# Kernel tuning notes

Measured on AMD Instinct MI355X. Metric: run time of the kernel, lower is better.

Reference implementation:

```python
import jax, jax.numpy as jnp
import numpy as np

EPS = 1e-5
MIN_NORM = 1e-10

def _norm(x):
    return jnp.sqrt(jnp.clip(jnp.sum(x * x, axis=-1, keepdims=True), MIN_NORM, None))

def _proj(x):
    # clip points to the open unit Poincare ball
    n = _norm(x)
    max_n = 1.0 - EPS
    return jnp.where(n > max_n, x * (max_n / n), x)

def _artanh(x):
    return jnp.arctanh(jnp.clip(x, -1.0 + EPS, 1.0 - EPS))

def mob_add(u, v):
    uv = jnp.sum(u * v, axis=-1, keepdims=True)
    u2 = jnp.sum(u * u, axis=-1, keepdims=True)
    v2 = jnp.sum(v * v, axis=-1, keepdims=True)
    num = (1.0 + 2.0 * uv + v2) * u + (1.0 - u2) * v
    den = 1.0 + 2.0 * uv + u2 * v2
    return _proj(num / jnp.maximum(den, MIN_NORM))

def mob_mat_mul(M, x):
    # M: [Din, Dout], x: [B, Din] on the ball. Ganea Mobius matvec.
    x = _proj(x)
    Mx = x @ M
    x_n = _norm(x)
    Mx_n = _norm(Mx)
    return _proj(jnp.tanh(Mx_n / x_n * _artanh(x_n)) * (Mx / Mx_n))

def log_map_zero(y):
    n = _norm(y)
    return _artanh(n) * y / n

def exp_map_zero(v):
    n = _norm(v)
    return _proj(jnp.tanh(n) * v / n)

def mob_pointwise_prod(x, u):
    # coordinate-wise scale of hyperbolic x by gate u, in the tangent space at 0
    return exp_map_zero(log_map_zero(x) * u)

def _transition(W, h, U, x, b):
    Wh = mob_mat_mul(W, h)
    Ux = mob_mat_mul(U, x)
    return mob_add(mob_add(Wh, Ux), b)

def setup_inputs() -> dict:
    B, I, H = 2048, 1024, 1024
    Din, Dh = 2 * I, 2 * H
    k = (1.0 / H) ** 0.5
    key = jax.random.key(0)
    ks = jax.random.split(key, 8)
    return {
        "hyp_x": jax.random.normal(ks[0], (B, Din), jnp.float32) * 0.01,
        "hidden": jax.random.normal(ks[1], (B, Dh), jnp.float32) * 0.01,
        "w_z": jax.random.uniform(ks[2], (Dh, Dh), jnp.float32, -k, k),
        "w_r": jax.random.uniform(ks[3], (Dh, Dh), jnp.float32, -k, k),
        "w_h": jax.random.uniform(ks[4], (Dh, Dh), jnp.float32, -k, k),
        "u_z": jax.random.uniform(ks[5], (Din, Dh), jnp.float32, -k, k),
        "u_r": jax.random.uniform(ks[6], (Din, Dh), jnp.float32, -k, k),
        "b_z": jnp.zeros((Dh,), jnp.float32),
        "b_r": jnp.zeros((Dh,), jnp.float32),
        "b_h": jnp.zeros((Dh,), jnp.float32),
    }

def reference(hyp_x, hidden, w_z, w_r, w_h, u_z, u_r, b_z, b_r, b_h):
    hyp_x = _proj(hyp_x)
    hidden = _proj(hidden)
    z = jax.nn.sigmoid(log_map_zero(_transition(w_z, hidden, u_z, hyp_x, b_z)))
    r = jax.nn.sigmoid(log_map_zero(_transition(w_r, hidden, u_r, hyp_x, b_r)))
    r_point_h = mob_pointwise_prod(hidden, r)
    # NOTE: original source uses u_r (not u_h) here; replicated faithfully.
    h_tilde = _transition(w_h, r_point_h, u_r, hyp_x, b_h)
    minus_h_oplus_htilde = mob_add(-hidden, h_tilde)
    new_h = mob_add(hidden, mob_pointwise_prod(minus_h_oplus_htilde, z))
    return new_h
```

## Files before the change

kernel.cpp:

```cpp
#include <hip/hip_runtime.h>
#include <hip/hip_bf16.h>
#include <math.h>

#define EPS 1e-5f
#define MAXN (1.0f - EPS)
#define MINN 1e-10f

constexpr int D = 2048;

typedef unsigned short u16;
typedef __bf16 bf16x8 __attribute__((ext_vector_type(8)));
typedef float floatx4 __attribute__((ext_vector_type(4)));


__device__ __forceinline__ u16 f2bf(float f) {
    union { float f; unsigned u; } v; v.f = f;
    unsigned r = v.u + 0x7FFFu + ((v.u >> 16) & 1u);
    return (u16)(r >> 16);
}

__device__ __forceinline__ float bf2f(u16 b) {
    union { unsigned u; float f; } v; v.u = ((unsigned)b) << 16; return v.f;
}

__device__ __forceinline__ void load_bf8(const u16* p, float* d) {
    uint4 r = *(const uint4*)p;
    unsigned w[4] = {r.x, r.y, r.z, r.w};
    #pragma unroll
    for (int i = 0; i < 4; ++i) {
        d[2 * i]     = bf2f((u16)(w[i] & 0xFFFFu));
        d[2 * i + 1] = bf2f((u16)(w[i] >> 16));
    }
}

__device__ __forceinline__ void store_bf8(u16* p, const float* s) {
    u16 pk[8];
    #pragma unroll
    for (int i = 0; i < 8; ++i) pk[i] = f2bf(s[i]);
    *(uint4*)p = *(const uint4*)pk;
}

__device__ __forceinline__ void load_f8(const float* p, float* d) {
    *(float4*)(d)     = *(const float4*)(p);
    *(float4*)(d + 4) = *(const float4*)(p + 4);
}

__device__ __forceinline__ void store_f8(float* p, const float* s) {
    *(float4*)(p)     = *(const float4*)(s);
    *(float4*)(p + 4) = *(const float4*)(s + 4);
}

__device__ __forceinline__ float artanh_(float x) {
    x = fminf(fmaxf(x, -1.0f + EPS), 1.0f - EPS);
    return 0.5f * logf((1.0f + x) / (1.0f - x));
}

__device__ __forceinline__ float sigmoid_(float x) {
    return 1.0f / (1.0f + expf(-x));
}

__device__ __forceinline__ void gl_lds16(const u16* g, u16* l) {
    __builtin_amdgcn_global_load_lds(
        (const __attribute__((address_space(1))) unsigned int*)g,
        (__attribute__((address_space(3))) unsigned int*)l, 16, 0, 0);
}

template<int N>
__device__ __forceinline__ void block_sums(float* v, float* sbuf) {
    #pragma unroll
    for (int n = 0; n < N; ++n)
        #pragma unroll
        for (int off = 32; off >= 1; off >>= 1) v[n] += __shfl_xor(v[n], off, 64);
    int w = threadIdx.x >> 6;
    __syncthreads();
    if ((threadIdx.x & 63) == 0) {
        #pragma unroll
        for (int n = 0; n < N; ++n) sbuf[w * N + n] = v[n];
    }
    __syncthreads();
    #pragma unroll
    for (int n = 0; n < N; ++n)
        v[n] = sbuf[n] + sbuf[N + n] + sbuf[2 * N + n] + sbuf[3 * N + n];
}

__device__ __forceinline__ void mmm_finish(float sum2, float g, float* coef, float* onorm) {
    float mxn = sqrtf(fmaxf(sum2, MINN));
    float tt  = tanhf(mxn * g);
    float on  = fminf(tt, MAXN);
    *coef = on / mxn;
    *onorm = on;
}

__device__ __forceinline__ float mob_apply(float* u, const float* v,
                                           float u2, float v2, float duv) {
    float cu  = 1.f + 2.f * duv + v2;
    float cv  = 1.f - u2;
    float den = fmaxf(1.f + 2.f * duv + u2 * v2, MINN);
    float s2  = cu * cu * u2 + 2.f * cu * cv * duv + cv * cv * v2;
    float n   = sqrtf(fmaxf(s2 / (den * den), MINN));
    float sc  = ((n > MAXN) ? MAXN / n : 1.f) / den;
    #pragma unroll
    for (int i = 0; i < 8; ++i) u[i] = sc * (cu * u[i] + cv * v[i]);
    return fminf(n, MAXN);
}

__device__ __forceinline__ void trans_tile(const float* W, u16* Wt,
                                           int n0, int k0, float* tile) {
    int t = threadIdx.x;
    int lr = t >> 4, lc = (t & 15) * 4;
    #pragma unroll
    for (int p = 0; p < 4; ++p) {
        int r = lr + p * 16;
        float4 v = *(const float4*)(W + (size_t)(k0 + r) * D + n0 + lc);
        tile[r * 65 + lc + 0] = v.x;
        tile[r * 65 + lc + 1] = v.y;
        tile[r * 65 + lc + 2] = v.z;
        tile[r * 65 + lc + 3] = v.w;
    }
    __syncthreads();
    int wn = t >> 3, ws = (t & 7) * 8;
    #pragma unroll
    for (int p = 0; p < 2; ++p) {
        int n = wn + p * 32;
        u16 pk[8];
        #pragma unroll
        for (int j = 0; j < 8; ++j) pk[j] = f2bf(tile[(ws + j) * 65 + n]);
        *(uint4*)(Wt + (size_t)(n0 + n) * D + k0 + ws) = *(uint4*)pk;
    }
}


struct PrepBatch {
    const float* W[5]; u16* Wt[5];
    const float* hx; const float* h;
    u16* hx_bf; u16* h_bf;
    float* g_x; float* g_h;
};

__global__ __launch_bounds__(256) void wtrans_prep(PrepBatch pb) {
    __shared__ float tile[64 * 65];
    int t = threadIdx.x;

    if (blockIdx.z != 4) {
        int wi = (blockIdx.z == 5) ? 4 : blockIdx.z;
        trans_tile(pb.W[wi], pb.Wt[wi],
                   blockIdx.x * 64, blockIdx.y * 64, tile);
    } else {
        int bid = blockIdx.y * (D / 64) + blockIdx.x;
        for (int rr = 0; rr < 2; ++rr) {
            int b = bid * 2 + rr;
            size_t off = (size_t)b * D + t * 8;
            float xv[8], hv[8];
            load_f8(pb.hx + off, xv);
            load_f8(pb.h + off, hv);
            float s[2] = {0.f, 0.f};
            #pragma unroll
            for (int i = 0; i < 8; ++i) { s[0] += xv[i] * xv[i]; s[1] += hv[i] * hv[i]; }
            block_sums<2>(s, tile);

            float nx = sqrtf(fmaxf(s[0], MINN));
            float scx = (nx > MAXN) ? MAXN / nx : 1.0f;
            float nh = sqrtf(fmaxf(s[1], MINN));
            float sch = (nh > MAXN) ? MAXN / nh : 1.0f;
            #pragma unroll
            for (int i = 0; i < 8; ++i) { xv[i] *= scx; hv[i] *= sch; }
            store_bf8(pb.hx_bf + off, xv);
            store_bf8(pb.h_bf + off, hv);
            if (t == 0) {
                float xn = fminf(nx, MAXN), hn = fminf(nh, MAXN);
                pb.g_x[b] = artanh_(xn) / xn;
                pb.g_h[b] = artanh_(hn) / hn;
            }
        }
    }
}


#define PHASE_MID() do { \
    __builtin_amdgcn_s_barrier(); \
    __builtin_amdgcn_s_setprio(1); } while (0)

#define PHASE_END() do { \
    __builtin_amdgcn_s_setprio(0); \
    __builtin_amdgcn_s_barrier(); } while (0)

template<int KLEN, int NJ>
__device__ __forceinline__ void gemm256_body(const u16* __restrict__ A,
                                             const u16* __restrict__ W,
                                             u16* __restrict__ C, int koff,
                                             u16* As, u16* Ws) {
    constexpr int T  = KLEN / 64;
    constexpr int BN = NJ * 64;
    constexpr int AU = 8192;
    constexpr int BU = BN * 32;

    int t0 = threadIdx.x;
    int wave = t0 >> 6, lane = t0 & 63, l16 = lane & 15, quad = lane >> 4;
    int wr = wave >> 2, wc = wave & 3;
    int brow = blockIdx.y * 256, bcol = blockIdx.x * BN;

    int srow = t0 >> 2;
    int sseg = (t0 & 3) ^ ((srow >> 1) & 3);
    const u16* srcA = A + (size_t)(brow + srow) * D + koff + sseg * 8;
    const u16* srcB = W + (size_t)(bcol + srow) * D + koff + sseg * 8;
    u16* ldsA = As + wave * 512;
    u16* ldsB = Ws + wave * 512;

    auto stageA = [&](int buf, int kh, int tile) {
        const u16* s = srcA + tile * 64 + kh * 32;
        u16* d = ldsA + (buf * 2 + kh) * AU;
        gl_lds16(s, d);
        gl_lds16(s + (size_t)128 * D, d + 4096);
    };
    auto stageB = [&](int buf, int kh, int tile) {
        const u16* s = srcB + tile * 64 + kh * 32;
        u16* d = ldsB + (buf * 2 + kh) * BU;
        gl_lds16(s, d);
        if constexpr (NJ == 4) gl_lds16(s + (size_t)128 * D, d + 4096);
    };

    const u16* aF = As + (wr * 128 + l16) * 32 + ((quad ^ ((l16 >> 1) & 3)) * 8);
    const u16* bF = Ws + (wc * (NJ * 16) + l16) * 32 + ((quad ^ ((l16 >> 1) & 3)) * 8);

    floatx4 acc[8][NJ];
    #pragma unroll
    for (int i = 0; i < 8; ++i)
        #pragma unroll
        for (int j = 0; j < NJ; ++j)
            #pragma unroll
            for (int e = 0; e < 4; ++e) acc[i][j][e] = 0.f;

    stageA(0, 0, 0); stageB(0, 0, 0);
    stageA(0, 1, 0); stageB(0, 1, 0);
    stageA(1, 0, 1); stageB(1, 0, 1);
    if constexpr (NJ == 4) asm volatile("s_waitcnt vmcnt(4)" ::: "memory");
    else                   asm volatile("s_waitcnt vmcnt(3)" ::: "memory");
    __builtin_amdgcn_s_barrier();

    #pragma unroll 2
    for (int tt = 0; tt < T; ++tt) {
        int bsel = tt & 1, bno = bsel ^ 1;
        const u16* aT = aF + bsel * (2 * AU);
        const u16* bT = bF + bsel * (2 * BU);
        bool st1 = (tt + 1) < T, st2 = (tt + 2) < T;

        bf16x8 bfr[NJ], afr[8];
        #pragma unroll
        for (int j = 0; j < NJ; ++j) bfr[j] = *(const bf16x8*)(bT + j * 512);
        #pragma unroll
        for (int i = 0; i < 8; ++i) afr[i] = *(const bf16x8*)(aT + i * 512);
        if (st1) { stageA(bno, 1, tt + 1); stageB(bno, 1, tt + 1); }
        PHASE_MID();
        #pragma unroll
        for (int i = 0; i < 8; ++i)
            #pragma unroll
            for (int j = 0; j < NJ; ++j)
                acc[i][j] = __builtin_amdgcn_mfma_f32_16x16x32_bf16(afr[i], bfr[j], acc[i][j], 0, 0, 0);
        PHASE_END();
        #pragma unroll
        for (int j = 0; j < NJ; ++j) bfr[j] = *(const bf16x8*)(bT + BU + j * 512);
        #pragma unroll
        for (int i = 0; i < 8; ++i) afr[i] = *(const bf16x8*)(aT + AU + i * 512);
        if (st2) { stageA(bsel, 0, tt + 2); stageB(bsel, 0, tt + 2); }
        PHASE_MID();
        #pragma unroll
        for (int i = 0; i < 8; ++i)
            #pragma unroll
            for (int j = 0; j < NJ; ++j)
                acc[i][j] = __builtin_amdgcn_mfma_f32_16x16x32_bf16(afr[i], bfr[j], acc[i][j], 0, 0, 0);
        __builtin_amdgcn_s_setprio(0);
        if constexpr (NJ == 4) asm volatile("s_waitcnt vmcnt(4)" ::: "memory");
        else                   asm volatile("s_waitcnt vmcnt(3)" ::: "memory");
        __builtin_amdgcn_s_barrier();
    }

    #pragma unroll
    for (int i = 0; i < 8; ++i) {
        #pragma unroll
        for (int j = 0; j < NJ; ++j) {
            int row = brow + wr * 128 + i * 16 + quad * 4;
            int col = bcol + wc * (NJ * 16) + j * 16 + l16;
            #pragma unroll
            for (int r = 0; r < 4; ++r)
                C[(size_t)(row + r) * D + col] = f2bf(acc[i][j][r]);
        }
    }
}


struct G1Batch { const u16* A[4]; const u16* W[4]; u16* C[4]; };

__global__ __launch_bounds__(512, 2) void g1_kernel(G1Batch gb) {
    __shared__ u16 As[32768];
    __shared__ u16 Ws[32768];
    int z = blockIdx.z;
    gemm256_body<2048, 4>(gb.A[z], gb.W[z], gb.C[z], 0, As, Ws);
}


struct GemmBatch { const u16* A[2]; const u16* W[2]; u16* C[2]; int koff[2]; };

__global__ __launch_bounds__(512, 2) void g2_kernel(GemmBatch gb) {
    __shared__ u16 As[32768];
    __shared__ u16 Ws[16384];
    int z = blockIdx.z;
    gemm256_body<1024, 2>(gb.A[z], gb.W[z], gb.C[z], gb.koff[z], As, Ws);
}


__global__ __launch_bounds__(256) void mid_kernel(
    const u16* __restrict__ c_wz, const u16* __restrict__ c_uz,
    const u16* __restrict__ c_wr, const u16* __restrict__ c_ur,
    const u16* __restrict__ h_bf,
    const float* __restrict__ g_x, const float* __restrict__ g_h,
    const float* __restrict__ b_z, const float* __restrict__ b_r,
    u16* __restrict__ z_out, u16* __restrict__ uxr_out,
    u16* __restrict__ rph_bf, float* __restrict__ g_rph) {
    __shared__ float sbuf[24];
    int b = blockIdx.x, t = threadIdx.x;
    size_t off = (size_t)b * D + t * 8;
    int cbase = t * 8;

    float wz[8], uz[8], wr2[8], ur2[8], hp[8], bz[8], br[8];
    load_bf8(c_wz + off, wz);
    load_bf8(c_uz + off, uz);
    load_bf8(c_wr + off, wr2);
    load_bf8(c_ur + off, ur2);
    load_bf8(h_bf + off, hp);
    load_f8(b_z + cbase, bz);
    load_f8(b_r + cbase, br);

    float s[6] = {0, 0, 0, 0, 0, 0};
    #pragma unroll
    for (int i = 0; i < 8; ++i) {
        s[0] += wz[i] * wz[i];  s[1] += uz[i] * uz[i];
        s[2] += wr2[i] * wr2[i]; s[3] += ur2[i] * ur2[i];
        s[4] += bz[i] * bz[i];  s[5] += br[i] * br[i];
    }
    block_sums<6>(s, sbuf);
    float gh = g_h[b], gx = g_x[b];

    float cwz, nwz, cuz, nuz, cwr, nwr, cur, nur;
    mmm_finish(s[0], gh, &cwz, &nwz);
    mmm_finish(s[1], gx, &cuz, &nuz);
    mmm_finish(s[2], gh, &cwr, &nwr);
    mmm_finish(s[3], gx, &cur, &nur);
    #pragma unroll
    for (int i = 0; i < 8; ++i) {
        wz[i] *= cwz; uz[i] *= cuz; wr2[i] *= cwr; ur2[i] *= cur;
    }
    float sbz = s[4], sbr2 = s[5];

    float d[2] = {0.f, 0.f};
    #pragma unroll
    for (int i = 0; i < 8; ++i) { d[0] += wz[i] * uz[i]; d[1] += wr2[i] * ur2[i]; }
    block_sums<2>(d, sbuf);
    float n1z = mob_apply(wz, uz, nwz * nwz, nuz * nuz, d[0]);
    float n1r = mob_apply(wr2, ur2, nwr * nwr, nur * nur, d[1]);

    d[0] = 0.f; d[1] = 0.f;
    #pragma unroll
    for (int i = 0; i < 8; ++i) { d[0] += wz[i] * bz[i]; d[1] += wr2[i] * br[i]; }
    block_sums<2>(d, sbuf);
    float n2z = mob_apply(wz, bz, n1z * n1z, sbz, d[0]);
    float n2r = mob_apply(wr2, br, n1r * n1r, sbr2, d[1]);

    float gz = artanh_(n2z) / n2z;
    float gr = artanh_(n2r) / n2r;
    float zz[8], v[8];
    float sv = 0.f;
    #pragma unroll
    for (int i = 0; i < 8; ++i) {
        zz[i] = sigmoid_(gz * wz[i]);
        float r = sigmoid_(gr * wr2[i]);
        v[i] = gh * hp[i] * r;
        sv += v[i] * v[i];
    }
    store_bf8(z_out + off, zz);
    block_sums<1>(&sv, sbuf);
    float nv = sqrtf(fmaxf(sv, MINN));
    float th = fminf(tanhf(nv), MAXN);
    float cr = th / nv;
    #pragma unroll
    for (int i = 0; i < 8; ++i) v[i] *= cr;
    store_bf8(rph_bf + off, v);
    store_bf8(uxr_out + off, ur2);
    if (t == 0) g_rph[b] = artanh_(th) / th;
}


__global__ __launch_bounds__(256) void fin_kernel(
    const u16* __restrict__ p0, const u16* __restrict__ p1,
    const u16* __restrict__ uxr, const u16* __restrict__ z_in,
    const u16* __restrict__ h_bf,
    const float* __restrict__ g_rph, const float* __restrict__ b_h,
    float* __restrict__ out) {
    __shared__ float sbuf[16];
    int b = blockIdx.x, t = threadIdx.x;
    size_t off = (size_t)b * D + t * 8;
    int cbase = t * 8;

    float wh[8], ux[8], zz[8], hp[8], bh[8], t0[8];
    load_bf8(p0 + off, wh);
    load_bf8(p1 + off, t0);
    #pragma unroll
    for (int i = 0; i < 8; ++i) wh[i] += t0[i];
    load_bf8(uxr + off, ux);
    load_bf8(z_in + off, zz);
    load_bf8(h_bf + off, hp);
    load_f8(b_h + cbase, bh);

    float s[4] = {0, 0, 0, 0};
    #pragma unroll
    for (int i = 0; i < 8; ++i) {
        s[0] += wh[i] * wh[i]; s[1] += ux[i] * ux[i];
        s[2] += hp[i] * hp[i]; s[3] += bh[i] * bh[i];
    }
    block_sums<4>(s, sbuf);
    float swh = s[0], sux = s[1], shp = s[2], sbh = s[3];

    float cwh, nwh;
    mmm_finish(swh, g_rph[b], &cwh, &nwh);
    #pragma unroll
    for (int i = 0; i < 8; ++i) wh[i] *= cwh;

    float d = 0.f;
    #pragma unroll
    for (int i = 0; i < 8; ++i) d += wh[i] * ux[i];
    block_sums<1>(&d, sbuf);
    float n1 = mob_apply(wh, ux, nwh * nwh, sux, d);

    d = 0.f;
    #pragma unroll
    for (int i = 0; i < 8; ++i) d += wh[i] * bh[i];
    block_sums<1>(&d, sbuf);
    float nht = mob_apply(wh, bh, n1 * n1, sbh, d);

    #pragma unroll
    for (int i = 0; i < 8; ++i) ux[i] = -hp[i];
    d = 0.f;
    #pragma unroll
    for (int i = 0; i < 8; ++i) d += ux[i] * wh[i];
    block_sums<1>(&d, sbuf);
    float nm = mob_apply(ux, wh, shp, nht * nht, d);

    float lm = artanh_(nm) / nm;
    float sv = 0.f;
    #pragma unroll
    for (int i = 0; i < 8; ++i) {
        float v = lm * ux[i] * zz[i];
        ux[i] = v;
        sv += v * v;
    }
    block_sums<1>(&sv, sbuf);
    float nv = sqrtf(fmaxf(sv, MINN));
    float th = fminf(tanhf(nv), MAXN);
    float ce = th / nv;
    #pragma unroll
    for (int i = 0; i < 8; ++i) ux[i] *= ce;

    d = 0.f;
    #pragma unroll
    for (int i = 0; i < 8; ++i) d += hp[i] * ux[i];
    block_sums<1>(&d, sbuf);
    mob_apply(hp, ux, shp, th * th, d);
    store_f8(out + off, hp);
}


extern "C" void kernel_launch(void* const* d_in, const int* in_sizes, int n_in,
                              void* d_out, int out_size, void* d_ws, size_t ws_size,
                              hipStream_t stream) {
    const float* hyp_x  = (const float*)d_in[0];
    const float* hidden = (const float*)d_in[1];
    const float* w_z = (const float*)d_in[2];
    const float* w_r = (const float*)d_in[3];
    const float* w_h = (const float*)d_in[4];
    const float* u_z = (const float*)d_in[5];
    const float* u_r = (const float*)d_in[6];
    const float* b_z = (const float*)d_in[7];
    const float* b_r = (const float*)d_in[8];
    const float* b_h = (const float*)d_in[9];
    float* out = (float*)d_out;

    int B = in_sizes[1] / D;

    char* ws = (char*)d_ws;
    size_t o = 0;
    auto alloc = [&](size_t bytes) -> void* {
        void* p = ws + o;
        o += (bytes + 255) & ~(size_t)255;
        return p;
    };
    u16* wt[5];
    for (int i = 0; i < 5; ++i) wt[i] = (u16*)alloc((size_t)D * D * 2);
    u16* hx_bf = (u16*)alloc((size_t)B * D * 2);
    u16* h_bf  = (u16*)alloc((size_t)B * D * 2);
    float* g_x   = (float*)alloc((size_t)B * 4);
    float* g_h   = (float*)alloc((size_t)B * 4);
    float* g_rph = (float*)alloc((size_t)B * 4);
    u16* cz0 = (u16*)alloc((size_t)B * D * 2);
    u16* cz1 = (u16*)alloc((size_t)B * D * 2);
    u16* cz2 = (u16*)alloc((size_t)B * D * 2);
    u16* cz3 = (u16*)alloc((size_t)B * D * 2);
    u16* z_buf = cz0;
    u16* uxr   = cz1;
    u16* rph   = cz2;
    u16* p0    = cz3;
    u16* p1    = hx_bf;

    PrepBatch pb;
    pb.W[0] = w_z; pb.Wt[0] = wt[0];
    pb.W[1] = w_r; pb.Wt[1] = wt[1];
    pb.W[2] = u_z; pb.Wt[2] = wt[3];
    pb.W[3] = u_r; pb.Wt[3] = wt[4];
    pb.W[4] = w_h; pb.Wt[4] = wt[2];
    pb.hx = hyp_x; pb.h = hidden;
    pb.hx_bf = hx_bf; pb.h_bf = h_bf;
    pb.g_x = g_x; pb.g_h = g_h;
    wtrans_prep<<<dim3(D / 64, D / 64, 6), 256, 0, stream>>>(pb);

    G1Batch g1;
    g1.A[0] = h_bf;  g1.W[0] = wt[0]; g1.C[0] = cz0;
    g1.A[1] = hx_bf; g1.W[1] = wt[3]; g1.C[1] = cz1;
    g1.A[2] = h_bf;  g1.W[2] = wt[1]; g1.C[2] = cz2;
    g1.A[3] = hx_bf; g1.W[3] = wt[4]; g1.C[3] = cz3;
    g1_kernel<<<dim3(D / 256, B / 256, 4), 512, 0, stream>>>(g1);

    mid_kernel<<<dim3(B), 256, 0, stream>>>(cz0, cz1, cz2, cz3, h_bf, g_x, g_h,
                                            b_z, b_r, z_buf, uxr, rph, g_rph);

    GemmBatch g2;
    g2.A[0] = rph; g2.W[0] = wt[2]; g2.C[0] = p0; g2.koff[0] = 0;
    g2.A[1] = rph; g2.W[1] = wt[2]; g2.C[1] = p1; g2.koff[1] = 1024;
    g2_kernel<<<dim3(D / 128, B / 256, 2), 512, 0, stream>>>(g2);

    fin_kernel<<<dim3(B), 256, 0, stream>>>(p0, p1, uxr, z_buf, h_bf,
                                            g_rph, b_h, out);
}
```

Before: 293.3 us.

## Remap GEMM blocks per XCD and split g2 into four K-chunks with 256x256 tiles

```diff
diff --git a/kernel.cpp b/kernel.cpp
--- a/kernel.cpp
+++ b/kernel.cpp
@@ -188,16 +188,15 @@
 __device__ __forceinline__ void gemm256_body(const u16* __restrict__ A,
                                              const u16* __restrict__ W,
                                              u16* __restrict__ C, int koff,
+                                             int brow, int bcol,
                                              u16* As, u16* Ws) {
     constexpr int T  = KLEN / 64;
-    constexpr int BN = NJ * 64;
     constexpr int AU = 8192;
-    constexpr int BU = BN * 32;
+    constexpr int BU = NJ * 64 * 32;
 
     int t0 = threadIdx.x;
     int wave = t0 >> 6, lane = t0 & 63, l16 = lane & 15, quad = lane >> 4;
     int wr = wave >> 2, wc = wave & 3;
-    int brow = blockIdx.y * 256, bcol = blockIdx.x * BN;
 
     int srow = t0 >> 2;
     int sseg = (t0 & 3) ^ ((srow >> 1) & 3);
@@ -287,24 +286,35 @@
     }
 }
 
+__device__ __forceinline__ int xcd_chunk256(void) {
+    int flat = blockIdx.x + (blockIdx.y << 3) + (blockIdx.z << 6);
+    return (flat & 7) * 32 + (flat >> 3);
+}
+
 
 struct G1Batch { const u16* A[4]; const u16* W[4]; u16* C[4]; };
 
 __global__ __launch_bounds__(512, 2) void g1_kernel(G1Batch gb) {
     __shared__ u16 As[32768];
     __shared__ u16 Ws[32768];
-    int z = blockIdx.z;
-    gemm256_body<2048, 4>(gb.A[z], gb.W[z], gb.C[z], 0, As, Ws);
-}
-
-
-struct GemmBatch { const u16* A[2]; const u16* W[2]; u16* C[2]; int koff[2]; };
+    int lid = xcd_chunk256();
+    int z = lid >> 6, rem = lid & 63;
+    int by = rem >> 3, bx = rem & 7;
+    gemm256_body<2048, 4>(gb.A[z], gb.W[z], gb.C[z], 0,
+                          by * 256, bx * 256, As, Ws);
+}
+
+
+struct GemmBatch { const u16* A; const u16* W; u16* C[4]; };
 
 __global__ __launch_bounds__(512, 2) void g2_kernel(GemmBatch gb) {
     __shared__ u16 As[32768];
-    __shared__ u16 Ws[16384];
-    int z = blockIdx.z;
-    gemm256_body<1024, 2>(gb.A[z], gb.W[z], gb.C[z], gb.koff[z], As, Ws);
+    __shared__ u16 Ws[32768];
+    int lid = xcd_chunk256();
+    int z = lid >> 6, rem = lid & 63;
+    int by = rem >> 3, bx = rem & 7;
+    gemm256_body<512, 4>(gb.A, gb.W, gb.C[z], z * 512,
+                         by * 256, bx * 256, As, Ws);
 }
 
 
@@ -391,6 +401,7 @@
 
 __global__ __launch_bounds__(256) void fin_kernel(
     const u16* __restrict__ p0, const u16* __restrict__ p1,
+    const u16* __restrict__ p2, const u16* __restrict__ p3,
     const u16* __restrict__ uxr, const u16* __restrict__ z_in,
     const u16* __restrict__ h_bf,
     const float* __restrict__ g_rph, const float* __restrict__ b_h,
@@ -403,6 +414,12 @@
     float wh[8], ux[8], zz[8], hp[8], bh[8], t0[8];
     load_bf8(p0 + off, wh);
     load_bf8(p1 + off, t0);
+    #pragma unroll
+    for (int i = 0; i < 8; ++i) wh[i] += t0[i];
+    load_bf8(p2 + off, t0);
+    #pragma unroll
+    for (int i = 0; i < 8; ++i) wh[i] += t0[i];
+    load_bf8(p3 + off, t0);
     #pragma unroll
     for (int i = 0; i < 8; ++i) wh[i] += t0[i];
     load_bf8(uxr + off, ux);
@@ -503,6 +520,8 @@
     u16* cz1 = (u16*)alloc((size_t)B * D * 2);
     u16* cz2 = (u16*)alloc((size_t)B * D * 2);
     u16* cz3 = (u16*)alloc((size_t)B * D * 2);
+    u16* p2  = (u16*)alloc((size_t)B * D * 2);
+    u16* p3  = (u16*)alloc((size_t)B * D * 2);
     u16* z_buf = cz0;
     u16* uxr   = cz1;
     u16* rph   = cz2;
@@ -525,16 +544,16 @@
     g1.A[1] = hx_bf; g1.W[1] = wt[3]; g1.C[1] = cz1;
     g1.A[2] = h_bf;  g1.W[2] = wt[1]; g1.C[2] = cz2;
     g1.A[3] = hx_bf; g1.W[3] = wt[4]; g1.C[3] = cz3;
-    g1_kernel<<<dim3(D / 256, B / 256, 4), 512, 0, stream>>>(g1);
+    g1_kernel<<<dim3(8, 8, 4), 512, 0, stream>>>(g1);
 
     mid_kernel<<<dim3(B), 256, 0, stream>>>(cz0, cz1, cz2, cz3, h_bf, g_x, g_h,
                                             b_z, b_r, z_buf, uxr, rph, g_rph);
 
     GemmBatch g2;
-    g2.A[0] = rph; g2.W[0] = wt[2]; g2.C[0] = p0; g2.koff[0] = 0;
-    g2.A[1] = rph; g2.W[1] = wt[2]; g2.C[1] = p1; g2.koff[1] = 1024;
-    g2_kernel<<<dim3(D / 128, B / 256, 2), 512, 0, stream>>>(g2);
-
-    fin_kernel<<<dim3(B), 256, 0, stream>>>(p0, p1, uxr, z_buf, h_bf,
+    g2.A = rph; g2.W = wt[2];
+    g2.C[0] = p0; g2.C[1] = p1; g2.C[2] = p2; g2.C[3] = p3;
+    g2_kernel<<<dim3(8, 8, 4), 512, 0, stream>>>(g2);
+
+    fin_kernel<<<dim3(B), 256, 0, stream>>>(p0, p1, p2, p3, uxr, z_buf, h_bf,
                                             g_rph, b_h, out);
 }
```

Result: no change. 297.4 us (+1.4%).
